# Kernel tuning notes

Hardware: AMD Instinct MI355X
Metric: run time of the kernel (lower is better)

Reference implementation:

```python
import jax, jax.numpy as jnp
import numpy as np

NUM_EXPERTS = 8
TOP_K = 2
ROUTED_SCALE = 1.0  # routed_scaling_factor
D_MODEL = 2048
D_FFN = 1408


def setup_inputs() -> dict:
    key = jax.random.key(0)
    ks = jax.random.split(key, 8)
    s = 0.02  # init scale for weights
    return {
        'hidden_states': jax.random.normal(ks[0], (2, 1024, D_MODEL), jnp.float32),
        'gate_w': jax.random.normal(ks[1], (NUM_EXPERTS, D_MODEL), jnp.float32) * s,
        'w_gate': jax.random.normal(ks[2], (NUM_EXPERTS, D_MODEL, D_FFN), jnp.float32) * s,
        'w_up': jax.random.normal(ks[3], (NUM_EXPERTS, D_MODEL, D_FFN), jnp.float32) * s,
        'w_down': jax.random.normal(ks[4], (NUM_EXPERTS, D_FFN, D_MODEL), jnp.float32) * s,
        'sw_gate': jax.random.normal(ks[5], (D_MODEL, D_FFN), jnp.float32) * s,
        'sw_up': jax.random.normal(ks[6], (D_MODEL, D_FFN), jnp.float32) * s,
        'sw_down': jax.random.normal(ks[7], (D_FFN, D_MODEL), jnp.float32) * s,
    }


def reference(hidden_states, gate_w, w_gate, w_up, w_down, sw_gate, sw_up, sw_down):
    B, S, D = hidden_states.shape
    x = hidden_states.reshape(-1, D)            # [T, D]
    T = x.shape[0]

    # --- router: fp32 linear -> softmax -> top-k -> renormalize ---
    logits = jnp.einsum('td,ed->te', x.astype(jnp.float32), gate_w)   # [T, E]
    probs = jax.nn.softmax(logits, axis=-1)
    topk_w, topk_ids = jax.lax.top_k(probs, TOP_K)                    # [T, K]
    topk_w = topk_w / jnp.sum(topk_w, axis=-1, keepdims=True)         # norm_topk_prob
    # dense per-token expert gates [T, E] (zero for unselected experts)
    gates = jnp.zeros((T, NUM_EXPERTS), jnp.float32).at[
        jnp.arange(T)[:, None], topk_ids].add(topk_w)
    gates = gates.astype(x.dtype)

    # --- routed experts: SwiGLU per expert, masked dense combine ---
    g = jnp.einsum('td,edf->etf', x, w_gate)    # [E, T, F]
    u = jnp.einsum('td,edf->etf', x, w_up)      # [E, T, F]
    h = jax.nn.silu(g) * u                      # SiluAndMul
    down = jnp.einsum('etf,efd->etd', h, w_down)  # [E, T, D]
    routed = jnp.einsum('te,etd->td', gates, down)  # combine
    routed = routed * ROUTED_SCALE

    # --- shared expert MLP ---
    shared = (jax.nn.silu(x @ sw_gate) * (x @ sw_up)) @ sw_down

    out = routed + shared
    return out.reshape(B, S, D)
```

## Files before the change

kernel.cpp:

```cpp
#include <hip/hip_runtime.h>
#include <hip/hip_bf16.h>

#define T_TOK 2048
#define DM    2048
#define FF    1408
#define NE    8
#define MT_ROUTED 40
#define MT_TOTAL  56
#define ROUTED_CAP 5120
#define NSLOT 7168

typedef unsigned short u16;
typedef __attribute__((ext_vector_type(4))) u16 u16x4;
typedef __attribute__((ext_vector_type(8))) u16 u16x8;
typedef __attribute__((ext_vector_type(8))) short bf16x8;
typedef __attribute__((ext_vector_type(4))) float f32x4;

__device__ __forceinline__ u16 f2bf(float f) {
    __hip_bfloat16 b = __float2bfloat16(f);
    union { __hip_bfloat16 b; u16 u; } cv;
    cv.b = b;
    return cv.u;
}
__device__ __forceinline__ float bf2f(u16 v) {
    return __uint_as_float(((unsigned)v) << 16);
}

__device__ __forceinline__ void gll16(const void* g, void* l) {
    __builtin_amdgcn_global_load_lds((const __attribute__((address_space(1))) void*)g,
                                     (__attribute__((address_space(3))) void*)l, 16, 0, 0);
}

constexpr size_t SZ_XB  = (size_t)T_TOK * DM * 2;
constexpr size_t SZ_WE  = (size_t)NE * DM * FF * 2;
constexpr size_t SZ_SW  = (size_t)DM * FF * 2;
constexpr size_t SZ_H   = (size_t)NSLOT * FF * 2;
constexpr size_t SZ_DN  = (size_t)NSLOT * DM * 2;

constexpr size_t OFF_XB   = 0;
constexpr size_t OFF_WGT  = OFF_XB + SZ_XB;
constexpr size_t OFF_WUT  = OFF_WGT + SZ_WE;
constexpr size_t OFF_WDT  = OFF_WUT + SZ_WE;
constexpr size_t OFF_SWG  = OFF_WDT + SZ_WE;
constexpr size_t OFF_SWU  = OFF_SWG + SZ_SW;
constexpr size_t OFF_SWD  = OFF_SWU + SZ_SW;
constexpr size_t OFF_H    = OFF_SWD + SZ_SW;
constexpr size_t OFF_DN   = OFF_H + SZ_H;
constexpr size_t OFF_TID  = OFF_DN + SZ_DN;
constexpr size_t OFF_TW   = OFF_TID + (size_t)T_TOK*2*4;
constexpr size_t OFF_PERM = OFF_TW  + (size_t)T_TOK*2*4;
constexpr size_t OFF_SW_S = OFF_PERM + (size_t)ROUTED_CAP*4;
constexpr size_t OFF_TKS  = OFF_SW_S + (size_t)ROUTED_CAP*4;
constexpr size_t OFF_TE   = OFF_TKS + (size_t)T_TOK*2*4;

__global__ __launch_bounds__(256, 4)
void tcvt_kernel(const float* __restrict__ wg, const float* __restrict__ wu,
                 const float* __restrict__ swg, const float* __restrict__ swu,
                 const float* __restrict__ wd, const float* __restrict__ swd,
                 u16* __restrict__ wgT, u16* __restrict__ wuT,
                 u16* __restrict__ swgT, u16* __restrict__ swuT,
                 u16* __restrict__ wdT, u16* __restrict__ swdT) {
    __shared__ u16x4 tile[2][2][64][16];
    const int z = blockIdx.z;
    const size_t msz = (size_t)DM * FF;
    const float* s; u16* d; int R, C, trow, tcol;
    if (z < 18) {
        R = DM; C = FF;
        trow = blockIdx.x / 11; tcol = blockIdx.x % 11;
        if (z < 8)       { s = wg + (size_t)z * msz;       d = wgT + (size_t)z * msz; }
        else if (z < 16) { s = wu + (size_t)(z - 8) * msz; d = wuT + (size_t)(z - 8) * msz; }
        else if (z == 16){ s = swg;                         d = swgT; }
        else             { s = swu;                         d = swuT; }
    } else {
        R = FF; C = DM;
        trow = blockIdx.x / 16; tcol = blockIdx.x % 16;
        if (z < 26) { s = wd + (size_t)(z - 18) * msz; d = wdT + (size_t)(z - 18) * msz; }
        else        { s = swd;                          d = swdT; }
    }
    const int r0 = trow * 128, c0 = tcol * 128;
    const int tid = threadIdx.x;
    const int rr = tid >> 5;
    const int c4 = tid & 31;
    const int cq = c4 >> 4, cc = c4 & 15;

#pragma unroll
    for (int h = 0; h < 2; h++) {
        float4 v[8];
#pragma unroll
        for (int i = 0; i < 8; i++) {
            const int r = h * 64 + i * 8 + rr;
            v[i] = *(const float4*)(s + (size_t)(r0 + r) * C + (c0 + c4 * 4));
        }
#pragma unroll
        for (int i = 0; i < 8; i++) {
            const int r = h * 64 + i * 8 + rr;
            u16x4 o;
            o[0] = f2bf(v[i].x); o[1] = f2bf(v[i].y);
            o[2] = f2bf(v[i].z); o[3] = f2bf(v[i].w);
            const int pr = ((((r >> 2) ^ ((r & 3) << 2)) & 15) ^ ((r & 64) >> 3));
            tile[r >> 6][cq][r & 63][cc ^ pr] = o;
        }
    }
    __syncthreads();

    const int oc = tid >> 4;
    const int rc = tid & 15;
    const int rq = rc >> 3, r7 = rc & 7;
#pragma unroll
    for (int j = 0; j < 8; j++) {
        const int c = j * 16 + oc;
        const int ch = (c >> 2) & 15, cl = c & 3, cq2 = c >> 6;
        u16x8 o;
#pragma unroll
        for (int k = 0; k < 8; k++) {
            const int rl = r7 * 8 + k;
            const int pr = ((((rl >> 2) ^ ((rl & 3) << 2)) & 15) ^ (rq << 3));
            o[k] = tile[rq][cq2][rl][ch ^ pr][cl];
        }
        *(u16x8*)(d + (size_t)(c0 + c) * R + (r0 + rc * 8)) = o;
    }
}

__global__ void router_kernel(const float* __restrict__ x, const float* __restrict__ gw,
                              u16* __restrict__ xb,
                              int* __restrict__ topk_id, float* __restrict__ topk_w) {
    const int wv = threadIdx.x >> 6, l = threadIdx.x & 63;
    const int t = blockIdx.x * 4 + wv;
    const float* xt = x + (size_t)t * DM;
    u16* xbt = xb + (size_t)t * DM;
    float acc[NE] = {0.f,0.f,0.f,0.f,0.f,0.f,0.f,0.f};
    for (int d = l * 4; d < DM; d += 256) {
        const float4 xv = *(const float4*)(xt + d);
        u16x4 o; o[0] = f2bf(xv.x); o[1] = f2bf(xv.y); o[2] = f2bf(xv.z); o[3] = f2bf(xv.w);
        *(u16x4*)(xbt + d) = o;
#pragma unroll
        for (int e = 0; e < NE; e++) {
            const float4 w4 = *(const float4*)(gw + e * DM + d);
            acc[e] += xv.x * w4.x + xv.y * w4.y + xv.z * w4.z + xv.w * w4.w;
        }
    }
#pragma unroll
    for (int e = 0; e < NE; e++)
#pragma unroll
        for (int off = 32; off > 0; off >>= 1) acc[e] += __shfl_xor(acc[e], off, 64);
    if (l == 0) {
        float m = acc[0];
#pragma unroll
        for (int e = 1; e < NE; e++) m = fmaxf(m, acc[e]);
        float p[NE];
#pragma unroll
        for (int e = 0; e < NE; e++) p[e] = __expf(acc[e] - m);
        int i1 = 0; float b1 = p[0];
#pragma unroll
        for (int e = 1; e < NE; e++) if (p[e] > b1) { b1 = p[e]; i1 = e; }
        int i2 = -1; float b2 = -1.f;
#pragma unroll
        for (int e = 0; e < NE; e++) if (e != i1 && p[e] > b2) { b2 = p[e]; i2 = e; }
        const float s = b1 + b2;
        topk_id[2*t] = i1; topk_id[2*t+1] = i2;
        topk_w[2*t] = b1 / s; topk_w[2*t+1] = b2 / s;
    }
}

__global__ void scan_kernel(const int* __restrict__ topk_id, const float* __restrict__ topk_w,
                            int* __restrict__ perm_token, float* __restrict__ slot_w,
                            int* __restrict__ tk_slot, int* __restrict__ tile_e) {
    const int e = blockIdx.x;
    const int tid = threadIdx.x;
    __shared__ int cnt[NE];
    __shared__ int tsum[256];
    int ids[16];
#pragma unroll
    for (int j = 0; j < 16; j++) ids[j] = topk_id[tid * 16 + j];
    if (tid < NE) cnt[tid] = 0;
    __syncthreads();
#pragma unroll
    for (int e2 = 0; e2 < NE; e2++) {
        int c = 0;
#pragma unroll
        for (int j = 0; j < 16; j++) c += (ids[j] == e2);
        if (c) atomicAdd(&cnt[e2], c);
    }
    int mySum = 0;
#pragma unroll
    for (int j = 0; j < 16; j++) mySum += (ids[j] == e);
    tsum[tid] = mySum;
    __syncthreads();
    if (tid == 0) { int run = 0; for (int i = 0; i < 256; i++) { int v = tsum[i]; tsum[i] = run; run += v; } }
    __syncthreads();
    int poff = 0;
#pragma unroll
    for (int e2 = 0; e2 < NE; e2++) { int p = (cnt[e2] + 127) & ~127; if (e2 < e) poff += p; }
    const int padded_e = (cnt[e] + 127) & ~127;
    int run = tsum[tid];
#pragma unroll
    for (int j = 0; j < 16; j++) {
        if (ids[j] == e) {
            const int i = tid * 16 + j;
            const int slot = poff + run;
            perm_token[slot] = i >> 1;
            slot_w[slot] = topk_w[i];
            tk_slot[i] = slot;
            run++;
        }
    }
    for (int r = cnt[e] + tid; r < padded_e; r += 256) { perm_token[poff + r] = 0; slot_w[poff + r] = 0.f; }
    if (tid == 0) for (int tt = poff >> 7; tt < (poff + padded_e) >> 7; tt++) tile_e[tt] = e;
    if (e == 0 && tid == 1) {
        int ptot = 0;
#pragma unroll
        for (int e2 = 0; e2 < NE; e2++) ptot += (cnt[e2] + 127) & ~127;
        for (int tt = ptot >> 7; tt < MT_ROUTED; tt++) tile_e[tt] = -1;
        for (int tt = MT_ROUTED; tt < MT_TOTAL; tt++) tile_e[tt] = 8;
    }
}

__global__ __launch_bounds__(256, 4)
void gemm1_kernel(const u16* __restrict__ xb,
                  const u16* __restrict__ wgT, const u16* __restrict__ wuT,
                  const u16* __restrict__ swgT, const u16* __restrict__ swuT,
                  const int* __restrict__ perm_token, const float* __restrict__ slot_w,
                  const int* __restrict__ tile_e, u16* __restrict__ hbuf) {
    const int bid = blockIdx.x;
    const int swz = (bid & 7) * 154 + (bid >> 3);
    const int mtile = swz % 56, ntile = swz / 56;
    const int e = tile_e[mtile];
    if (e < 0) return;
    __shared__ u16 lA[128 * 64], lB[128 * 64];
    __shared__ int lTok[128];
    __shared__ float lW[128];
    const int tid = threadIdx.x, l = tid & 63, w = tid >> 6;
    const bool sh = (e == 8);
    const int slot_base = sh ? (ROUTED_CAP + (mtile - MT_ROUTED) * 128) : mtile * 128;
    if (tid < 128) {
        if (sh) { lTok[tid] = (mtile - MT_ROUTED) * 128 + tid; lW[tid] = 1.0f; }
        else    { lTok[tid] = perm_token[slot_base + tid]; lW[tid] = slot_w[slot_base + tid]; }
    }
    __syncthreads();
    const u16* Bg = sh ? swgT : (wgT + (size_t)e * FF * DM);
    const u16* Bu = sh ? swuT : (wuT + (size_t)e * FF * DM);
    const int n0 = ntile * 64;
    const u16* aSrc[4]; const u16* bSrc[4]; int ldsOff[4];
#pragma unroll
    for (int i = 0; i < 4; i++) {
        const int row = i * 32 + w * 8 + (l >> 3);
        const int ch = (l & 7) ^ (row & 7);
        ldsOff[i] = (i * 32 + w * 8) * 64;
        aSrc[i] = xb + (size_t)lTok[row] * DM + ch * 8;
        const u16* bbase = (i < 2) ? (Bg + (size_t)(n0 + row) * DM)
                                   : (Bu + (size_t)(n0 + row - 64) * DM);
        bSrc[i] = bbase + ch * 8;
    }
    f32x4 acc[2][8] = {};
    const int wm = w * 32;
    for (int k0 = 0; k0 < DM; k0 += 64) {
        __syncthreads();
#pragma unroll
        for (int i = 0; i < 4; i++) { gll16(aSrc[i] + k0, lA + ldsOff[i]); gll16(bSrc[i] + k0, lB + ldsOff[i]); }
        __syncthreads();
#pragma unroll
        for (int kk = 0; kk < 64; kk += 32) {
            bf16x8 af[2], bf_[8];
#pragma unroll
            for (int mi = 0; mi < 2; mi++) {
                const int row = wm + mi * 16 + (l & 15);
                const int ch = ((kk >> 3) + (l >> 4)) ^ (row & 7);
                af[mi] = *(const bf16x8*)(lA + row * 64 + ch * 8);
            }
#pragma unroll
            for (int ni = 0; ni < 8; ni++) {
                const int row = ni * 16 + (l & 15);
                const int ch = ((kk >> 3) + (l >> 4)) ^ (row & 7);
                bf_[ni] = *(const bf16x8*)(lB + row * 64 + ch * 8);
            }
#pragma unroll
            for (int mi = 0; mi < 2; mi++)
#pragma unroll
                for (int ni = 0; ni < 8; ni++)
                    acc[mi][ni] = __builtin_amdgcn_mfma_f32_16x16x32_bf16(af[mi], bf_[ni], acc[mi][ni], 0, 0, 0);
        }
    }
#pragma unroll
    for (int mi = 0; mi < 2; mi++)
#pragma unroll
        for (int r = 0; r < 4; r++) {
            const int m = wm + mi * 16 + (l >> 4) * 4 + r;
            const float wgt = lW[m];
#pragma unroll
            for (int ni = 0; ni < 4; ni++) {
                const int n = ni * 16 + (l & 15);
                const float g = acc[mi][ni][r], u = acc[mi][ni + 4][r];
                const float h = g * (1.f / (1.f + __expf(-g))) * u * wgt;
                hbuf[(size_t)(slot_base + m) * FF + n0 + n] = f2bf(h);
            }
        }
}

__global__ __launch_bounds__(256, 5)
void gemm2_kernel(const u16* __restrict__ hbuf, const u16* __restrict__ wdT,
                  const u16* __restrict__ swdT, const int* __restrict__ tile_e,
                  u16* __restrict__ dn) {
    const int bid = blockIdx.x;
    const int swz = (bid & 7) * 224 + (bid >> 3);
    const int mtile = swz % 56, ntile = swz / 56;
    const int e = tile_e[mtile];
    if (e < 0) return;
    __shared__ u16 lA[128 * 64], lB[64 * 64];
    const int tid = threadIdx.x, l = tid & 63, w = tid >> 6;
    const bool sh = (e == 8);
    const int slot_base = sh ? (ROUTED_CAP + (mtile - MT_ROUTED) * 128) : mtile * 128;
    const u16* Bp = sh ? swdT : (wdT + (size_t)e * DM * FF);
    const int n0 = ntile * 64;
    const u16* aSrc[4]; const u16* bSrc[2]; int aOff[4], bOff[2];
#pragma unroll
    for (int i = 0; i < 4; i++) {
        const int row = i * 32 + w * 8 + (l >> 3);
        const int ch = (l & 7) ^ (row & 7);
        aOff[i] = (i * 32 + w * 8) * 64;
        aSrc[i] = hbuf + (size_t)(slot_base + row) * FF + ch * 8;
    }
#pragma unroll
    for (int i = 0; i < 2; i++) {
        const int row = i * 32 + w * 8 + (l >> 3);
        const int ch = (l & 7) ^ (row & 7);
        bOff[i] = (i * 32 + w * 8) * 64;
        bSrc[i] = Bp + (size_t)(n0 + row) * FF + ch * 8;
    }
    f32x4 acc[2][4] = {};
    const int wm = w * 32;
    for (int k0 = 0; k0 < FF; k0 += 64) {
        __syncthreads();
#pragma unroll
        for (int i = 0; i < 4; i++) gll16(aSrc[i] + k0, lA + aOff[i]);
#pragma unroll
        for (int i = 0; i < 2; i++) gll16(bSrc[i] + k0, lB + bOff[i]);
        __syncthreads();
#pragma unroll
        for (int kk = 0; kk < 64; kk += 32) {
            bf16x8 af[2], bf_[4];
#pragma unroll
            for (int mi = 0; mi < 2; mi++) {
                const int row = wm + mi * 16 + (l & 15);
                const int ch = ((kk >> 3) + (l >> 4)) ^ (row & 7);
                af[mi] = *(const bf16x8*)(lA + row * 64 + ch * 8);
            }
#pragma unroll
            for (int ni = 0; ni < 4; ni++) {
                const int row = ni * 16 + (l & 15);
                const int ch = ((kk >> 3) + (l >> 4)) ^ (row & 7);
                bf_[ni] = *(const bf16x8*)(lB + row * 64 + ch * 8);
            }
#pragma unroll
            for (int mi = 0; mi < 2; mi++)
#pragma unroll
                for (int ni = 0; ni < 4; ni++)
                    acc[mi][ni] = __builtin_amdgcn_mfma_f32_16x16x32_bf16(af[mi], bf_[ni], acc[mi][ni], 0, 0, 0);
        }
    }
#pragma unroll
    for (int mi = 0; mi < 2; mi++)
#pragma unroll
        for (int r = 0; r < 4; r++) {
            const int m = wm + mi * 16 + (l >> 4) * 4 + r;
#pragma unroll
            for (int ni = 0; ni < 4; ni++) {
                const int n = ni * 16 + (l & 15);
                dn[(size_t)(slot_base + m) * DM + n0 + n] = f2bf(acc[mi][ni][r]);
            }
        }
}

__global__ void combine_kernel(const u16* __restrict__ dn, const int* __restrict__ tk_slot,
                               float* __restrict__ out) {
    const int i = blockIdx.x * 256 + threadIdx.x;
    const int base = i * 8;
    const int t = base >> 11, d = base & 2047;
    const int s1 = tk_slot[2 * t], s2 = tk_slot[2 * t + 1];
    const bf16x8 a = *(const bf16x8*)(dn + (size_t)s1 * DM + d);
    const bf16x8 b = *(const bf16x8*)(dn + (size_t)s2 * DM + d);
    const bf16x8 c = *(const bf16x8*)(dn + (size_t)(ROUTED_CAP + t) * DM + d);
    float o[8];
#pragma unroll
    for (int j = 0; j < 8; j++)
        o[j] = bf2f((u16)a[j]) + bf2f((u16)b[j]) + bf2f((u16)c[j]);
    float4 lo, hi;
    lo.x = o[0]; lo.y = o[1]; lo.z = o[2]; lo.w = o[3];
    hi.x = o[4]; hi.y = o[5]; hi.z = o[6]; hi.w = o[7];
    *(float4*)(out + base) = lo;
    *(float4*)(out + base + 4) = hi;
}

extern "C" void kernel_launch(void* const* d_in, const int* in_sizes, int n_in,
                              void* d_out, int out_size, void* d_ws, size_t ws_size,
                              hipStream_t stream) {
    (void)in_sizes; (void)n_in; (void)out_size; (void)ws_size;
    const float* x   = (const float*)d_in[0];
    const float* gw  = (const float*)d_in[1];
    const float* wg  = (const float*)d_in[2];
    const float* wu  = (const float*)d_in[3];
    const float* wd  = (const float*)d_in[4];
    const float* swg = (const float*)d_in[5];
    const float* swu = (const float*)d_in[6];
    const float* swd = (const float*)d_in[7];
    float* out = (float*)d_out;
    char* ws = (char*)d_ws;

    u16*   xb    = (u16*)(ws + OFF_XB);
    u16*   wgT   = (u16*)(ws + OFF_WGT);
    u16*   wuT   = (u16*)(ws + OFF_WUT);
    u16*   wdT   = (u16*)(ws + OFF_WDT);
    u16*   swgT  = (u16*)(ws + OFF_SWG);
    u16*   swuT  = (u16*)(ws + OFF_SWU);
    u16*   swdT  = (u16*)(ws + OFF_SWD);
    u16*   hbuf  = (u16*)(ws + OFF_H);
    u16*   dn    = (u16*)(ws + OFF_DN);
    int*   tid_  = (int*)(ws + OFF_TID);
    float* tw    = (float*)(ws + OFF_TW);
    int*   perm  = (int*)(ws + OFF_PERM);
    float* slw   = (float*)(ws + OFF_SW_S);
    int*   tks   = (int*)(ws + OFF_TKS);
    int*   te    = (int*)(ws + OFF_TE);

    router_kernel<<<T_TOK / 4, 256, 0, stream>>>(x, gw, xb, tid_, tw);
    scan_kernel<<<NE, 256, 0, stream>>>(tid_, tw, perm, slw, tks, te);
    tcvt_kernel<<<dim3(176, 1, 27), 256, 0, stream>>>(wg, wu, swg, swu, wd, swd,
                                                      wgT, wuT, swgT, swuT, wdT, swdT);
    gemm1_kernel<<<1232, 256, 0, stream>>>(xb, wgT, wuT, swgT, swuT, perm, slw, te, hbuf);
    gemm2_kernel<<<1792, 256, 0, stream>>>(hbuf, wdT, swdT, te, dn);
    combine_kernel<<<(T_TOK * DM / 8) / 256, 256, 0, stream>>>(dn, tks, out);
}
```

Baseline: 321.9 us.

## Fuse fp32 gate/up weight conversion into gemm1, dropping separate transpose pass

The separate transpose-and-convert pass over the gate and up weights is removed. gemm1 now loads the fp32 weights directly into LDS, converts them to bf16 in shared memory, and runs 256-row M tiles with 512-thread blocks and a K step of 32. Routed padding grows to 256 rows, with gemm2's tile mapping and buffer sizes adjusted to match. This avoids writing and re-reading the bf16 gate/up weight copies, but it adds an extra LDS conversion pass and a barrier inside gemm1's main loop. The float-to-bf16 rounding is also replaced with a manual bit trick.

```diff
diff --git a/kernel.cpp b/kernel.cpp
--- a/kernel.cpp
+++ b/kernel.cpp
@@ -5,10 +5,12 @@
 #define DM    2048
 #define FF    1408
 #define NE    8
-#define MT_ROUTED 40
-#define MT_TOTAL  56
-#define ROUTED_CAP 5120
-#define NSLOT 7168
+#define ROUTED_CAP 6144
+#define NSLOT 8192
+#define MT1_ROUTED 24
+#define MT1_TOTAL  32
+#define MT2_ROUTED 48
+#define MT2_TOTAL  64
 
 typedef unsigned short u16;
 typedef __attribute__((ext_vector_type(4))) u16 u16x4;
@@ -17,10 +19,9 @@
 typedef __attribute__((ext_vector_type(4))) float f32x4;
 
 __device__ __forceinline__ u16 f2bf(float f) {
-    __hip_bfloat16 b = __float2bfloat16(f);
-    union { __hip_bfloat16 b; u16 u; } cv;
-    cv.b = b;
-    return cv.u;
+    unsigned u = __float_as_uint(f);
+    unsigned r = (u + 0x7FFFu + ((u >> 16) & 1u)) >> 16;
+    return (u16)r;
 }
 __device__ __forceinline__ float bf2f(u16 v) {
     return __uint_as_float(((unsigned)v) << 16);
@@ -32,19 +33,15 @@
 }
 
 constexpr size_t SZ_XB  = (size_t)T_TOK * DM * 2;
-constexpr size_t SZ_WE  = (size_t)NE * DM * FF * 2;
-constexpr size_t SZ_SW  = (size_t)DM * FF * 2;
+constexpr size_t SZ_WDT = (size_t)NE * DM * FF * 2;
+constexpr size_t SZ_SWD = (size_t)DM * FF * 2;
 constexpr size_t SZ_H   = (size_t)NSLOT * FF * 2;
 constexpr size_t SZ_DN  = (size_t)NSLOT * DM * 2;
 
 constexpr size_t OFF_XB   = 0;
-constexpr size_t OFF_WGT  = OFF_XB + SZ_XB;
-constexpr size_t OFF_WUT  = OFF_WGT + SZ_WE;
-constexpr size_t OFF_WDT  = OFF_WUT + SZ_WE;
-constexpr size_t OFF_SWG  = OFF_WDT + SZ_WE;
-constexpr size_t OFF_SWU  = OFF_SWG + SZ_SW;
-constexpr size_t OFF_SWD  = OFF_SWU + SZ_SW;
-constexpr size_t OFF_H    = OFF_SWD + SZ_SW;
+constexpr size_t OFF_WDT  = OFF_XB + SZ_XB;
+constexpr size_t OFF_SWD  = OFF_WDT + SZ_WDT;
+constexpr size_t OFF_H    = OFF_SWD + SZ_SWD;
 constexpr size_t OFF_DN   = OFF_H + SZ_H;
 constexpr size_t OFF_TID  = OFF_DN + SZ_DN;
 constexpr size_t OFF_TW   = OFF_TID + (size_t)T_TOK*2*4;
@@ -54,35 +51,21 @@
 constexpr size_t OFF_TE   = OFF_TKS + (size_t)T_TOK*2*4;
 
 __global__ __launch_bounds__(256, 4)
-void tcvt_kernel(const float* __restrict__ wg, const float* __restrict__ wu,
-                 const float* __restrict__ swg, const float* __restrict__ swu,
-                 const float* __restrict__ wd, const float* __restrict__ swd,
-                 u16* __restrict__ wgT, u16* __restrict__ wuT,
-                 u16* __restrict__ swgT, u16* __restrict__ swuT,
+void tcvt_kernel(const float* __restrict__ wd, const float* __restrict__ swd,
                  u16* __restrict__ wdT, u16* __restrict__ swdT) {
     __shared__ u16x4 tile[2][2][64][16];
     const int z = blockIdx.z;
     const size_t msz = (size_t)DM * FF;
-    const float* s; u16* d; int R, C, trow, tcol;
-    if (z < 18) {
-        R = DM; C = FF;
-        trow = blockIdx.x / 11; tcol = blockIdx.x % 11;
-        if (z < 8)       { s = wg + (size_t)z * msz;       d = wgT + (size_t)z * msz; }
-        else if (z < 16) { s = wu + (size_t)(z - 8) * msz; d = wuT + (size_t)(z - 8) * msz; }
-        else if (z == 16){ s = swg;                         d = swgT; }
-        else             { s = swu;                         d = swuT; }
-    } else {
-        R = FF; C = DM;
-        trow = blockIdx.x / 16; tcol = blockIdx.x % 16;
-        if (z < 26) { s = wd + (size_t)(z - 18) * msz; d = wdT + (size_t)(z - 18) * msz; }
-        else        { s = swd;                          d = swdT; }
-    }
+    const float* s; u16* d;
+    if (z < 8) { s = wd + (size_t)z * msz; d = wdT + (size_t)z * msz; }
+    else       { s = swd;                  d = swdT; }
+    const int R = FF, C = DM;
+    const int trow = blockIdx.x / 16, tcol = blockIdx.x % 16;
     const int r0 = trow * 128, c0 = tcol * 128;
     const int tid = threadIdx.x;
     const int rr = tid >> 5;
     const int c4 = tid & 31;
     const int cq = c4 >> 4, cc = c4 & 15;
-
 #pragma unroll
     for (int h = 0; h < 2; h++) {
         float4 v[8];
@@ -102,7 +85,6 @@
         }
     }
     __syncthreads();
-
     const int oc = tid >> 4;
     const int rc = tid & 15;
     const int rq = rc >> 3, r7 = rc & 7;
@@ -190,8 +172,8 @@
     __syncthreads();
     int poff = 0;
 #pragma unroll
-    for (int e2 = 0; e2 < NE; e2++) { int p = (cnt[e2] + 127) & ~127; if (e2 < e) poff += p; }
-    const int padded_e = (cnt[e] + 127) & ~127;
+    for (int e2 = 0; e2 < NE; e2++) { int p = (cnt[e2] + 255) & ~255; if (e2 < e) poff += p; }
+    const int padded_e = (cnt[e] + 255) & ~255;
     int run = tsum[tid];
 #pragma unroll
     for (int j = 0; j < 16; j++) {
@@ -209,75 +191,91 @@
     if (e == 0 && tid == 1) {
         int ptot = 0;
 #pragma unroll
-        for (int e2 = 0; e2 < NE; e2++) ptot += (cnt[e2] + 127) & ~127;
-        for (int tt = ptot >> 7; tt < MT_ROUTED; tt++) tile_e[tt] = -1;
-        for (int tt = MT_ROUTED; tt < MT_TOTAL; tt++) tile_e[tt] = 8;
-    }
-}
-
-__global__ __launch_bounds__(256, 4)
+        for (int e2 = 0; e2 < NE; e2++) ptot += (cnt[e2] + 255) & ~255;
+        for (int tt = ptot >> 7; tt < MT2_ROUTED; tt++) tile_e[tt] = -1;
+        for (int tt = MT2_ROUTED; tt < MT2_TOTAL; tt++) tile_e[tt] = 8;
+    }
+}
+
+__global__ __launch_bounds__(512, 6)
 void gemm1_kernel(const u16* __restrict__ xb,
-                  const u16* __restrict__ wgT, const u16* __restrict__ wuT,
-                  const u16* __restrict__ swgT, const u16* __restrict__ swuT,
+                  const float* __restrict__ wg, const float* __restrict__ wu,
+                  const float* __restrict__ swg, const float* __restrict__ swu,
                   const int* __restrict__ perm_token, const float* __restrict__ slot_w,
                   const int* __restrict__ tile_e, u16* __restrict__ hbuf) {
     const int bid = blockIdx.x;
-    const int swz = (bid & 7) * 154 + (bid >> 3);
-    const int mtile = swz % 56, ntile = swz / 56;
-    const int e = tile_e[mtile];
+    const int swz = (bid & 7) * 88 + (bid >> 3);
+    const int mtile = swz & 31, ntile = swz >> 5;
+    const int e = tile_e[mtile * 2];
     if (e < 0) return;
-    __shared__ u16 lA[128 * 64], lB[128 * 64];
-    __shared__ int lTok[128];
-    __shared__ float lW[128];
+    __shared__ u16 lA[128 * 64];
+    __shared__ u16 lB[64 * 64];
+    __shared__ float bf32[2][32][64];
+    __shared__ int lTok[256];
+    __shared__ float lW[256];
     const int tid = threadIdx.x, l = tid & 63, w = tid >> 6;
     const bool sh = (e == 8);
-    const int slot_base = sh ? (ROUTED_CAP + (mtile - MT_ROUTED) * 128) : mtile * 128;
-    if (tid < 128) {
-        if (sh) { lTok[tid] = (mtile - MT_ROUTED) * 128 + tid; lW[tid] = 1.0f; }
+    const int slot_base = sh ? (ROUTED_CAP + (mtile - MT1_ROUTED) * 256) : mtile * 256;
+    if (tid < 256) {
+        if (sh) { lTok[tid] = (mtile - MT1_ROUTED) * 256 + tid; lW[tid] = 1.0f; }
         else    { lTok[tid] = perm_token[slot_base + tid]; lW[tid] = slot_w[slot_base + tid]; }
     }
     __syncthreads();
-    const u16* Bg = sh ? swgT : (wgT + (size_t)e * FF * DM);
-    const u16* Bu = sh ? swuT : (wuT + (size_t)e * FF * DM);
+    const float* Bg = sh ? swg : (wg + (size_t)e * DM * FF);
+    const float* Bu = sh ? swu : (wu + (size_t)e * DM * FF);
     const int n0 = ntile * 64;
-    const u16* aSrc[4]; const u16* bSrc[4]; int ldsOff[4];
-#pragma unroll
-    for (int i = 0; i < 4; i++) {
-        const int row = i * 32 + w * 8 + (l >> 3);
-        const int ch = (l & 7) ^ (row & 7);
-        ldsOff[i] = (i * 32 + w * 8) * 64;
-        aSrc[i] = xb + (size_t)lTok[row] * DM + ch * 8;
-        const u16* bbase = (i < 2) ? (Bg + (size_t)(n0 + row) * DM)
-                                   : (Bu + (size_t)(n0 + row - 64) * DM);
-        bSrc[i] = bbase + ch * 8;
-    }
-    f32x4 acc[2][8] = {};
+
+    const int ci1 = w * 64 + l, ci2 = 512 + w * 64 + l;
+    const int m1 = (ci1 >> 3) * 2 + ((ci1 & 7) >> 2), kc1 = ci1 & 3;
+    const int m2 = (ci2 >> 3) * 2 + ((ci2 & 7) >> 2), kc2 = ci2 & 3;
+    const u16* aSrc1 = xb + (size_t)lTok[m1] * DM + kc1 * 8;
+    const u16* aSrc2 = xb + (size_t)lTok[m2] * DM + kc2 * 8;
+    u16* aDst1 = lA + w * 512;
+    u16* aDst2 = lA + 4096 + w * 512;
+    const int bk = w * 4 + (l >> 4), bc = (l & 15) * 4;
+    const float* bgSrc = Bg + (size_t)bk * FF + n0 + bc;
+    const float* buSrc = Bu + (size_t)bk * FF + n0 + bc;
+    float* bgDst = &bf32[0][0][0] + w * 256;
+    float* buDst = &bf32[1][0][0] + w * 256;
+    const int s2T = w >> 2, s2kq = w & 3;
+    const int s2pos = (((s2T << 2) + s2kq) ^ (l & 7)) * 8;
+
+    f32x4 accg[2][4] = {}; f32x4 accu[2][4] = {};
     const int wm = w * 32;
-    for (int k0 = 0; k0 < DM; k0 += 64) {
+
+    for (int k0 = 0; k0 < DM; k0 += 32) {
         __syncthreads();
-#pragma unroll
-        for (int i = 0; i < 4; i++) { gll16(aSrc[i] + k0, lA + ldsOff[i]); gll16(bSrc[i] + k0, lB + ldsOff[i]); }
+        gll16(aSrc1 + k0, aDst1);
+        gll16(aSrc2 + k0, aDst2);
+        gll16(bgSrc + (size_t)k0 * FF, bgDst);
+        gll16(buSrc + (size_t)k0 * FF, buDst);
         __syncthreads();
-#pragma unroll
-        for (int kk = 0; kk < 64; kk += 32) {
-            bf16x8 af[2], bf_[8];
+        {
+            float f[8];
+#pragma unroll
+            for (int i = 0; i < 8; i++) f[i] = bf32[s2T][s2kq * 8 + i][l];
+            u16x8 o;
+#pragma unroll
+            for (int i = 0; i < 8; i++) o[i] = f2bf(f[i]);
+            *(u16x8*)(lB + l * 64 + s2pos) = o;
+        }
+        __syncthreads();
+        bf16x8 af[2];
+#pragma unroll
+        for (int mi = 0; mi < 2; mi++) {
+            const int m = wm + mi * 16 + (l & 15);
+            af[mi] = *(const bf16x8*)(lA + (m >> 1) * 64 + (((m & 1) * 4 + (l >> 4)) * 8));
+        }
+#pragma unroll
+        for (int ni = 0; ni < 4; ni++) {
+            const int n = ni * 16 + (l & 15);
+            const bf16x8 bg = *(const bf16x8*)(lB + n * 64 + (((l >> 4) ^ (n & 7)) * 8));
+            const bf16x8 bu = *(const bf16x8*)(lB + n * 64 + (((4 + (l >> 4)) ^ (n & 7)) * 8));
 #pragma unroll
             for (int mi = 0; mi < 2; mi++) {
-                const int row = wm + mi * 16 + (l & 15);
-                const int ch = ((kk >> 3) + (l >> 4)) ^ (row & 7);
-                af[mi] = *(const bf16x8*)(lA + row * 64 + ch * 8);
+                accg[mi][ni] = __builtin_amdgcn_mfma_f32_16x16x32_bf16(af[mi], bg, accg[mi][ni], 0, 0, 0);
+                accu[mi][ni] = __builtin_amdgcn_mfma_f32_16x16x32_bf16(af[mi], bu, accu[mi][ni], 0, 0, 0);
             }
-#pragma unroll
-            for (int ni = 0; ni < 8; ni++) {
-                const int row = ni * 16 + (l & 15);
-                const int ch = ((kk >> 3) + (l >> 4)) ^ (row & 7);
-                bf_[ni] = *(const bf16x8*)(lB + row * 64 + ch * 8);
-            }
-#pragma unroll
-            for (int mi = 0; mi < 2; mi++)
-#pragma unroll
-                for (int ni = 0; ni < 8; ni++)
-                    acc[mi][ni] = __builtin_amdgcn_mfma_f32_16x16x32_bf16(af[mi], bf_[ni], acc[mi][ni], 0, 0, 0);
         }
     }
 #pragma unroll
@@ -289,7 +287,7 @@
 #pragma unroll
             for (int ni = 0; ni < 4; ni++) {
                 const int n = ni * 16 + (l & 15);
-                const float g = acc[mi][ni][r], u = acc[mi][ni + 4][r];
+                const float g = accg[mi][ni][r], u = accu[mi][ni][r];
                 const float h = g * (1.f / (1.f + __expf(-g))) * u * wgt;
                 hbuf[(size_t)(slot_base + m) * FF + n0 + n] = f2bf(h);
             }
@@ -301,14 +299,14 @@
                   const u16* __restrict__ swdT, const int* __restrict__ tile_e,
                   u16* __restrict__ dn) {
     const int bid = blockIdx.x;
-    const int swz = (bid & 7) * 224 + (bid >> 3);
-    const int mtile = swz % 56, ntile = swz / 56;
+    const int swz = (bid & 7) * 256 + (bid >> 3);
+    const int mtile = swz % 64, ntile = swz / 64;
     const int e = tile_e[mtile];
     if (e < 0) return;
     __shared__ u16 lA[128 * 64], lB[64 * 64];
     const int tid = threadIdx.x, l = tid & 63, w = tid >> 6;
     const bool sh = (e == 8);
-    const int slot_base = sh ? (ROUTED_CAP + (mtile - MT_ROUTED) * 128) : mtile * 128;
+    const int slot_base = sh ? (ROUTED_CAP + (mtile - MT2_ROUTED) * 128) : mtile * 128;
     const u16* Bp = sh ? swdT : (wdT + (size_t)e * DM * FF);
     const int n0 = ntile * 64;
     const u16* aSrc[4]; const u16* bSrc[2]; int aOff[4], bOff[2];
@@ -406,11 +404,7 @@
     char* ws = (char*)d_ws;
 
     u16*   xb    = (u16*)(ws + OFF_XB);
-    u16*   wgT   = (u16*)(ws + OFF_WGT);
-    u16*   wuT   = (u16*)(ws + OFF_WUT);
     u16*   wdT   = (u16*)(ws + OFF_WDT);
-    u16*   swgT  = (u16*)(ws + OFF_SWG);
-    u16*   swuT  = (u16*)(ws + OFF_SWU);
     u16*   swdT  = (u16*)(ws + OFF_SWD);
     u16*   hbuf  = (u16*)(ws + OFF_H);
     u16*   dn    = (u16*)(ws + OFF_DN);
@@ -423,9 +417,8 @@
 
     router_kernel<<<T_TOK / 4, 256, 0, stream>>>(x, gw, xb, tid_, tw);
     scan_kernel<<<NE, 256, 0, stream>>>(tid_, tw, perm, slw, tks, te);
-    tcvt_kernel<<<dim3(176, 1, 27), 256, 0, stream>>>(wg, wu, swg, swu, wd, swd,
-                                                      wgT, wuT, swgT, swuT, wdT, swdT);
-    gemm1_kernel<<<1232, 256, 0, stream>>>(xb, wgT, wuT, swgT, swuT, perm, slw, te, hbuf);
-    gemm2_kernel<<<1792, 256, 0, stream>>>(hbuf, wdT, swdT, te, dn);
+    tcvt_kernel<<<dim3(176, 1, 9), 256, 0, stream>>>(wd, swd, wdT, swdT);
+    gemm1_kernel<<<704, 512, 0, stream>>>(xb, wg, wu, swg, swu, perm, slw, te, hbuf);
+    gemm2_kernel<<<2048, 256, 0, stream>>>(hbuf, wdT, swdT, te, dn);
     combine_kernel<<<(T_TOK * DM / 8) / 256, 256, 0, stream>>>(dn, tks, out);
 }
```

After: 793.1 us. +146.4%, slower.
